# Optimization experiments

Measured on AMD Instinct MI355X. Metric: run time of the kernel, lower is better.

The kernel has to match this reference:

```python
import jax, jax.numpy as jnp
import numpy as np

B, N, F_IN, E_DIM, F, T = 4, 64, 32, 32, 64, 3


def setup_inputs() -> dict:
    key = jax.random.key(0)
    ks = jax.random.split(key, 8)
    X = jax.random.normal(ks[0], (B, N, F_IN), jnp.float32)
    # adjacency mask over the dense N*N ordered-pair layout, broadcast dim 1
    A = (jax.random.uniform(ks[1], (B, N * N, 1)) < 0.25).astype(jnp.float32)
    E = jax.random.normal(ks[2], (B, N * N, E_DIM), jnp.float32)

    def glorot(k, shape):
        fan_in, fan_out = shape
        lim = np.sqrt(6.0 / (fan_in + fan_out)).astype(np.float32)
        return jax.random.uniform(k, shape, jnp.float32, -lim, lim)

    W_embed = glorot(ks[3], (F_IN, F))
    b_embed = jnp.zeros((F,), jnp.float32)
    W_edge = glorot(ks[4], (E_DIM, F * F))
    b_edge = jnp.zeros((F * F,), jnp.float32)
    gru_k = glorot(ks[5], (F, 3 * F))        # input kernel  [F, 3F] (z|r|h)
    gru_rk = glorot(ks[6], (F, 3 * F))       # recurrent kernel
    gru_b = jnp.zeros((3 * F,), jnp.float32)   # input bias
    gru_rb = jnp.zeros((3 * F,), jnp.float32)  # recurrent bias (reset_after)
    return {"X": X, "A": A, "E": E, "W_embed": W_embed, "b_embed": b_embed,
            "W_edge": W_edge, "b_edge": b_edge, "gru_k": gru_k,
            "gru_rk": gru_rk, "gru_b": gru_b, "gru_rb": gru_rb}


def _gru_step(h, x, Wk, Uk, b, rb):
    # Keras GRU cell, reset_after=True: gate order z, r, h
    xg = x @ Wk + b
    hg = h @ Uk + rb
    xz, xr, xh = jnp.split(xg, 3, axis=-1)
    hz, hr, hh = jnp.split(hg, 3, axis=-1)
    z = jax.nn.sigmoid(xz + hz)
    r = jax.nn.sigmoid(xr + hr)
    cand = jnp.tanh(xh + r * hh)
    return z * h + (1.0 - z) * cand


def reference(X, A, E, W_embed, b_embed, W_edge, b_edge,
              gru_k, gru_rk, gru_b, gru_rb):
    H = jax.nn.relu(X @ W_embed + b_embed)            # [B,N,F]
    mask = A.reshape(B, N, N, 1)                      # adjacency mask
    # per-edge transformation matrices (E is constant across T rounds,
    # so the edge MLP is hoisted out of the loop -- same math as original)
    Amat = jax.nn.relu(E @ W_edge + b_edge).reshape(B, N, N, F, F)
    for _ in range(T):
        # message for target i from source j: A_{ij} @ H_j  (batched matvec)
        msgs = jnp.einsum('bnmij,bmj->bnmi', Amat, H)  # [B,N,N,F]
        agg = jnp.sum(msgs * mask, axis=2)             # [B,N,F]
        # GRU over the length-2 sequence [old_state, agg_messages], h0 = 0
        h = jnp.zeros_like(H)
        h = _gru_step(h, H, gru_k, gru_rk, gru_b, gru_rb)
        H = _gru_step(h, agg, gru_k, gru_rk, gru_b, gru_rb)
    return H
```

## Files before the change

kernel.cpp:

```cpp
#include <hip/hip_runtime.h>
#include <math.h>

#define Bv   4
#define Nv   64
#define FIN  32
#define EDIM 32
#define Fv   64
#define NN   (Nv*Nv)
#define ZROW 256

typedef __bf16 bf16x8 __attribute__((ext_vector_type(8)));
typedef float  f32x4  __attribute__((ext_vector_type(4)));

__device__ __forceinline__ float sigmoidf_(float x) {
    return 1.f / (1.f + __expf(-x));
}

__global__ __launch_bounds__(64) void prep_kernel(
    const float* __restrict__ X, const float* __restrict__ W_embed,
    const float* __restrict__ b_embed, const float* __restrict__ A,
    const float* __restrict__ E, const float* __restrict__ W_edge,
    float* __restrict__ H0, float* __restrict__ H1,
    __bf16* __restrict__ Wf, __bf16* __restrict__ Ebf,
    int* __restrict__ ml_g, int* __restrict__ cnt_g)
{
    const int blk  = blockIdx.x;
    const int lane = threadIdx.x;

    if (blk < 256) {
        const int nt = blk;
        const int kb = (lane >> 4) * 8;
        const int c  = nt*16 + (lane & 15);
        bf16x8 v;
        #pragma unroll
        for (int t = 0; t < 8; ++t)
            v[t] = (__bf16)W_edge[(kb + t)*4096 + c];
        *(bf16x8*)(Wf + ((size_t)(nt*64 + lane))*8) = v;
        if (blk == 0) {
            H0[ZROW*Fv + lane] = 0.f;
            H1[ZROW*Fv + lane] = 0.f;
        }
    } else if (blk < 512) {
        const int bn = blk - 256;
        const int b  = bn >> 6;
        const int n  = bn & 63;
        __shared__ int ml[Nv];

        const float av = A[b*NN + n*Nv + lane];
        const unsigned long long mk = __ballot(av != 0.f);
        const int cnt = (int)__popcll(mk);
        if (av != 0.f) {
            const int pos = (int)__popcll(mk & ((1ull << lane) - 1ull));
            ml[pos] = lane;
        }
        __syncthreads();

        ml_g[bn*64 + lane] = (lane < cnt) ? (b*Nv + ml[lane]) : ZROW;
        if (lane == 0) cnt_g[bn] = cnt;

        __bf16 row[EDIM];
        if (lane < cnt) {
            const float* er = E + ((size_t)(b*NN + n*Nv + ml[lane]))*EDIM;
            #pragma unroll
            for (int t = 0; t < 8; ++t) {
                const float4 x = *(const float4*)(er + 4*t);
                row[4*t  ] = (__bf16)x.x; row[4*t+1] = (__bf16)x.y;
                row[4*t+2] = (__bf16)x.z; row[4*t+3] = (__bf16)x.w;
            }
        } else {
            #pragma unroll
            for (int e = 0; e < EDIM; ++e) row[e] = (__bf16)0.f;
        }
        __bf16* dst = Ebf + ((size_t)(bn*64 + lane))*EDIM;
        #pragma unroll
        for (int t = 0; t < 4; ++t)
            *(bf16x8*)(dst + 8*t) = *(bf16x8*)(row + 8*t);
    } else {
        const int bn = blk - 512;
        __shared__ float xs[FIN];
        if (lane < FIN) xs[lane] = X[bn*FIN + lane];
        __syncthreads();
        float acc = b_embed[lane];
        #pragma unroll
        for (int k = 0; k < FIN; ++k)
            acc = fmaf(xs[k], W_embed[k*Fv + lane], acc);
        H0[bn*Fv + lane] = fmaxf(acc, 0.f);
    }
}

template<int MTN>
__device__ __forceinline__ void msg_body(
    int bn, int qq, int w, int lane,
    const float* __restrict__ Hin, const __bf16* __restrict__ Wf,
    const float* __restrict__ b_edge, const __bf16* __restrict__ Ebf,
    const int* __restrict__ ml_g, float* __restrict__ agg_g)
{
    const int c16 = lane & 15;
    const int rg  = (lane >> 4) * 4;
    const int kb  = (lane >> 4) * 8;

    bf16x8 af[MTN];
    int4   ri[MTN];
    #pragma unroll
    for (int mt = 0; mt < MTN; ++mt) {
        af[mt] = *(const bf16x8*)(Ebf + ((size_t)(bn*64 + mt*16 + c16))*EDIM + kb);
        ri[mt] = *(const int4*)(ml_g + bn*64 + mt*16 + rg);
    }

    const int i0 = qq*8 + w*2;
    float p0 = 0.f, p1 = 0.f;

    #pragma unroll
    for (int u = 0; u < 4; ++u) {
        const int jc = u*16 + c16;
        float hu[MTN][4];
        #pragma unroll
        for (int mt = 0; mt < MTN; ++mt) {
            hu[mt][0] = Hin[ri[mt].x*Fv + jc];
            hu[mt][1] = Hin[ri[mt].y*Fv + jc];
            hu[mt][2] = Hin[ri[mt].z*Fv + jc];
            hu[mt][3] = Hin[ri[mt].w*Fv + jc];
        }
        #pragma unroll
        for (int ii = 0; ii < 2; ++ii) {
            const int nt = (i0 + ii)*4 + u;
            const bf16x8 bf = *(const bf16x8*)(Wf + ((size_t)(nt*64 + lane))*8);
            const float  be = b_edge[nt*16 + c16];
            f32x4 cb; cb[0] = be; cb[1] = be; cb[2] = be; cb[3] = be;
            float acc = 0.f;
            #pragma unroll
            for (int mt = 0; mt < MTN; ++mt) {
                f32x4 d = __builtin_amdgcn_mfma_f32_16x16x32_bf16(af[mt], bf, cb, 0, 0, 0);
                acc = fmaf(fmaxf(d[0], 0.f), hu[mt][0], acc);
                acc = fmaf(fmaxf(d[1], 0.f), hu[mt][1], acc);
                acc = fmaf(fmaxf(d[2], 0.f), hu[mt][2], acc);
                acc = fmaf(fmaxf(d[3], 0.f), hu[mt][3], acc);
            }
            if (ii == 0) p0 += acc; else p1 += acc;
        }
    }
    #pragma unroll
    for (int off = 32; off > 0; off >>= 1) {
        p0 += __shfl_xor(p0, off);
        p1 += __shfl_xor(p1, off);
    }
    if (lane == 0) {
        agg_g[bn*Fv + i0]     = p0;
        agg_g[bn*Fv + i0 + 1] = p1;
    }
}

__global__ __launch_bounds__(256) void msg_kernel(
    const float* __restrict__ Hin, const __bf16* __restrict__ Wf,
    const float* __restrict__ b_edge, const __bf16* __restrict__ Ebf,
    const int* __restrict__ ml_g, const int* __restrict__ cnt_g,
    float* __restrict__ agg_g)
{
    const int bn   = blockIdx.x;
    const int qq   = blockIdx.y;
    const int tid  = threadIdx.x;
    const int w    = tid >> 6;
    const int lane = tid & 63;

    const int cnt = cnt_g[bn];
    const int Mt  = (cnt == 0) ? 1 : ((cnt + 15) >> 4);

    if (Mt <= 1) {
        msg_body<1>(bn, qq, w, lane, Hin, Wf, b_edge, Ebf, ml_g, agg_g);
    } else if (Mt == 2) {
        msg_body<2>(bn, qq, w, lane, Hin, Wf, b_edge, Ebf, ml_g, agg_g);
    } else {
        const int c16 = lane & 15;
        const int rg  = (lane >> 4) * 4;
        const int kb  = (lane >> 4) * 8;
        const int i0  = qq*8 + w*2;
        #pragma unroll
        for (int ii = 0; ii < 2; ++ii) {
            float part = 0.f;
            #pragma unroll 1
            for (int u = 0; u < 4; ++u) {
                const int jc = u*16 + c16;
                const int nt = (i0 + ii)*4 + u;
                const bf16x8 bf = *(const bf16x8*)(Wf + ((size_t)(nt*64 + lane))*8);
                const float  be = b_edge[nt*16 + c16];
                f32x4 cb; cb[0] = be; cb[1] = be; cb[2] = be; cb[3] = be;
                for (int mt = 0; mt < Mt; ++mt) {
                    const bf16x8 a_ = *(const bf16x8*)(Ebf + ((size_t)(bn*64 + mt*16 + c16))*EDIM + kb);
                    const int4 ri = *(const int4*)(ml_g + bn*64 + mt*16 + rg);
                    f32x4 d = __builtin_amdgcn_mfma_f32_16x16x32_bf16(a_, bf, cb, 0, 0, 0);
                    part = fmaf(fmaxf(d[0], 0.f), Hin[ri.x*Fv + jc], part);
                    part = fmaf(fmaxf(d[1], 0.f), Hin[ri.y*Fv + jc], part);
                    part = fmaf(fmaxf(d[2], 0.f), Hin[ri.z*Fv + jc], part);
                    part = fmaf(fmaxf(d[3], 0.f), Hin[ri.w*Fv + jc], part);
                }
            }
            #pragma unroll
            for (int off = 32; off > 0; off >>= 1)
                part += __shfl_xor(part, off);
            if (lane == 0) agg_g[bn*Fv + i0 + ii] = part;
        }
    }
}

__global__ __launch_bounds__(192) void gru_kernel(
    const float* __restrict__ Hin, const float* __restrict__ agg_g,
    float* __restrict__ Hout,
    const float* __restrict__ gk, const float* __restrict__ grk,
    const float* __restrict__ gb, const float* __restrict__ grb)
{
    const int bn  = blockIdx.x;
    const int tid = threadIdx.x;

    __shared__ float h_old[Fv];
    __shared__ float aggs[Fv];
    __shared__ float h1[Fv];
    __shared__ float xg[3*Fv];
    __shared__ float hg[3*Fv];

    if (tid < Fv) {
        h_old[tid] = Hin[bn*Fv + tid];
        aggs[tid]  = agg_g[bn*Fv + tid];
    }
    __syncthreads();

    {
        float a0 = 0.f, a1 = 0.f, a2 = 0.f, a3 = 0.f;
        #pragma unroll
        for (int k = 0; k < 16; ++k) {
            a0 = fmaf(h_old[k],      gk[(k     )*192 + tid], a0);
            a1 = fmaf(h_old[k + 16], gk[(k + 16)*192 + tid], a1);
            a2 = fmaf(h_old[k + 32], gk[(k + 32)*192 + tid], a2);
            a3 = fmaf(h_old[k + 48], gk[(k + 48)*192 + tid], a3);
        }
        xg[tid] = gb[tid] + ((a0 + a1) + (a2 + a3));
    }
    __syncthreads();
    if (tid < Fv) {
        float z    = sigmoidf_(xg[tid]       + grb[tid]);
        float r    = sigmoidf_(xg[64 + tid]  + grb[64 + tid]);
        float cand = tanhf    (xg[128 + tid] + r * grb[128 + tid]);
        h1[tid] = (1.f - z) * cand;
    }
    __syncthreads();

    {
        float x0 = 0.f, x1 = 0.f, x2 = 0.f, x3 = 0.f;
        float y0 = 0.f, y1 = 0.f, y2 = 0.f, y3 = 0.f;
        #pragma unroll
        for (int k = 0; k < 16; ++k) {
            x0 = fmaf(aggs[k],      gk [(k     )*192 + tid], x0);
            x1 = fmaf(aggs[k + 16], gk [(k + 16)*192 + tid], x1);
            x2 = fmaf(aggs[k + 32], gk [(k + 32)*192 + tid], x2);
            x3 = fmaf(aggs[k + 48], gk [(k + 48)*192 + tid], x3);
            y0 = fmaf(h1[k],        grk[(k     )*192 + tid], y0);
            y1 = fmaf(h1[k + 16],   grk[(k + 16)*192 + tid], y1);
            y2 = fmaf(h1[k + 32],   grk[(k + 32)*192 + tid], y2);
            y3 = fmaf(h1[k + 48],   grk[(k + 48)*192 + tid], y3);
        }
        xg[tid] = gb[tid]  + ((x0 + x1) + (x2 + x3));
        hg[tid] = grb[tid] + ((y0 + y1) + (y2 + y3));
    }
    __syncthreads();
    if (tid < Fv) {
        float z    = sigmoidf_(xg[tid]       + hg[tid]);
        float r    = sigmoidf_(xg[64 + tid]  + hg[64 + tid]);
        float cand = tanhf    (xg[128 + tid] + r * hg[128 + tid]);
        Hout[bn*Fv + tid] = z * h1[tid] + (1.f - z) * cand;
    }
}

extern "C" void kernel_launch(void* const* d_in, const int* in_sizes, int n_in,
                              void* d_out, int out_size, void* d_ws, size_t ws_size,
                              hipStream_t stream)
{
    const float* X       = (const float*)d_in[0];
    const float* A       = (const float*)d_in[1];
    const float* E       = (const float*)d_in[2];
    const float* W_embed = (const float*)d_in[3];
    const float* b_embed = (const float*)d_in[4];
    const float* W_edge  = (const float*)d_in[5];
    const float* b_edge  = (const float*)d_in[6];
    const float* gk      = (const float*)d_in[7];
    const float* grk     = (const float*)d_in[8];
    const float* gb      = (const float*)d_in[9];
    const float* grb     = (const float*)d_in[10];
    float* out = (float*)d_out;

    float*  H0  = (float*)d_ws;
    float*  H1  = H0 + (ZROW + 1)*Fv;
    __bf16* Wf  = (__bf16*)(H1 + (ZROW + 1)*Fv);
    __bf16* Ebf = Wf + 256*64*8;
    int*    ml_g  = (int*)(Ebf + (size_t)Bv*Nv*64*EDIM);
    int*    cnt_g = ml_g + Bv*Nv*64;

    const dim3 mgrid(Bv*Nv, 8);

    prep_kernel<<<768, 64, 0, stream>>>(X, W_embed, b_embed, A, E, W_edge,
                                        H0, H1, Wf, Ebf, ml_g, cnt_g);

    msg_kernel<<<mgrid, 256, 0, stream>>>(H0, Wf, b_edge, Ebf, ml_g, cnt_g, out);
    gru_kernel<<<Bv*Nv, 192, 0, stream>>>(H0, out, H1, gk, grk, gb, grb);
    msg_kernel<<<mgrid, 256, 0, stream>>>(H1, Wf, b_edge, Ebf, ml_g, cnt_g, out);
    gru_kernel<<<Bv*Nv, 192, 0, stream>>>(H1, out, H0, gk, grk, gb, grb);
    msg_kernel<<<mgrid, 256, 0, stream>>>(H0, Wf, b_edge, Ebf, ml_g, cnt_g, H1);
    gru_kernel<<<Bv*Nv, 192, 0, stream>>>(H0, H1, out, gk, grk, gb, grb);
}
```

Before: 48.09 us.

## Process two nodes per msg block and stage edge-weight fragments in LDS

```diff
diff --git a/kernel.cpp b/kernel.cpp
--- a/kernel.cpp
+++ b/kernel.cpp
@@ -45,7 +45,6 @@
         const int b  = bn >> 6;
         const int n  = bn & 63;
         __shared__ int ml[Nv];
-
         const float av = A[b*NN + n*Nv + lane];
         const unsigned long long mk = __ballot(av != 0.f);
         const int cnt = (int)__popcll(mk);
@@ -54,10 +53,8 @@
             ml[pos] = lane;
         }
         __syncthreads();
-
         ml_g[bn*64 + lane] = (lane < cnt) ? (b*Nv + ml[lane]) : ZROW;
         if (lane == 0) cnt_g[bn] = cnt;
-
         __bf16 row[EDIM];
         if (lane < cnt) {
             const float* er = E + ((size_t)(b*NN + n*Nv + ml[lane]))*EDIM;
@@ -89,9 +86,9 @@
 }
 
 template<int MTN>
-__device__ __forceinline__ void msg_body(
-    int bn, int qq, int w, int lane,
-    const float* __restrict__ Hin, const __bf16* __restrict__ Wf,
+__device__ __forceinline__ void msg_node_lds(
+    int bn, int i0, int lane,
+    const float* __restrict__ Hin, const __bf16* __restrict__ wfl,
     const float* __restrict__ b_edge, const __bf16* __restrict__ Ebf,
     const int* __restrict__ ml_g, float* __restrict__ agg_g)
 {
@@ -107,7 +104,6 @@
         ri[mt] = *(const int4*)(ml_g + bn*64 + mt*16 + rg);
     }
 
-    const int i0 = qq*8 + w*2;
     float p0 = 0.f, p1 = 0.f;
 
     #pragma unroll
@@ -123,8 +119,9 @@
         }
         #pragma unroll
         for (int ii = 0; ii < 2; ++ii) {
-            const int nt = (i0 + ii)*4 + u;
-            const bf16x8 bf = *(const bf16x8*)(Wf + ((size_t)(nt*64 + lane))*8);
+            const int nt  = (i0 + ii)*4 + u;
+            const int ntl = ii*4 + u;
+            const bf16x8 bf = *(const bf16x8*)(wfl + (ntl*64 + lane)*8);
             const float  be = b_edge[nt*16 + c16];
             f32x4 cb; cb[0] = be; cb[1] = be; cb[2] = be; cb[3] = be;
             float acc = 0.f;
@@ -150,56 +147,78 @@
     }
 }
 
+__device__ __forceinline__ void msg_general(
+    int bn, int Mt, int i0, int lane,
+    const float* __restrict__ Hin, const __bf16* __restrict__ Wf,
+    const float* __restrict__ b_edge, const __bf16* __restrict__ Ebf,
+    const int* __restrict__ ml_g, float* __restrict__ agg_g)
+{
+    const int c16 = lane & 15;
+    const int rg  = (lane >> 4) * 4;
+    const int kb  = (lane >> 4) * 8;
+    #pragma unroll
+    for (int ii = 0; ii < 2; ++ii) {
+        float part = 0.f;
+        #pragma unroll 1
+        for (int u = 0; u < 4; ++u) {
+            const int jc = u*16 + c16;
+            const int nt = (i0 + ii)*4 + u;
+            const bf16x8 bf = *(const bf16x8*)(Wf + ((size_t)(nt*64 + lane))*8);
+            const float  be = b_edge[nt*16 + c16];
+            f32x4 cb; cb[0] = be; cb[1] = be; cb[2] = be; cb[3] = be;
+            for (int mt = 0; mt < Mt; ++mt) {
+                const bf16x8 a_ = *(const bf16x8*)(Ebf + ((size_t)(bn*64 + mt*16 + c16))*EDIM + kb);
+                const int4 ri = *(const int4*)(ml_g + bn*64 + mt*16 + rg);
+                f32x4 d = __builtin_amdgcn_mfma_f32_16x16x32_bf16(a_, bf, cb, 0, 0, 0);
+                part = fmaf(fmaxf(d[0], 0.f), Hin[ri.x*Fv + jc], part);
+                part = fmaf(fmaxf(d[1], 0.f), Hin[ri.y*Fv + jc], part);
+                part = fmaf(fmaxf(d[2], 0.f), Hin[ri.z*Fv + jc], part);
+                part = fmaf(fmaxf(d[3], 0.f), Hin[ri.w*Fv + jc], part);
+            }
+        }
+        #pragma unroll
+        for (int off = 32; off > 0; off >>= 1)
+            part += __shfl_xor(part, off);
+        if (lane == 0) agg_g[bn*Fv + i0 + ii] = part;
+    }
+}
+
 __global__ __launch_bounds__(256) void msg_kernel(
     const float* __restrict__ Hin, const __bf16* __restrict__ Wf,
     const float* __restrict__ b_edge, const __bf16* __restrict__ Ebf,
     const int* __restrict__ ml_g, const int* __restrict__ cnt_g,
     float* __restrict__ agg_g)
 {
-    const int bn   = blockIdx.x;
+    const int g    = blockIdx.x;
     const int qq   = blockIdx.y;
     const int tid  = threadIdx.x;
     const int w    = tid >> 6;
     const int lane = tid & 63;
 
-    const int cnt = cnt_g[bn];
-    const int Mt  = (cnt == 0) ? 1 : ((cnt + 15) >> 4);
-
-    if (Mt <= 1) {
-        msg_body<1>(bn, qq, w, lane, Hin, Wf, b_edge, Ebf, ml_g, agg_g);
-    } else if (Mt == 2) {
-        msg_body<2>(bn, qq, w, lane, Hin, Wf, b_edge, Ebf, ml_g, agg_g);
-    } else {
-        const int c16 = lane & 15;
-        const int rg  = (lane >> 4) * 4;
-        const int kb  = (lane >> 4) * 8;
-        const int i0  = qq*8 + w*2;
-        #pragma unroll
-        for (int ii = 0; ii < 2; ++ii) {
-            float part = 0.f;
-            #pragma unroll 1
-            for (int u = 0; u < 4; ++u) {
-                const int jc = u*16 + c16;
-                const int nt = (i0 + ii)*4 + u;
-                const bf16x8 bf = *(const bf16x8*)(Wf + ((size_t)(nt*64 + lane))*8);
-                const float  be = b_edge[nt*16 + c16];
-                f32x4 cb; cb[0] = be; cb[1] = be; cb[2] = be; cb[3] = be;
-                for (int mt = 0; mt < Mt; ++mt) {
-                    const bf16x8 a_ = *(const bf16x8*)(Ebf + ((size_t)(bn*64 + mt*16 + c16))*EDIM + kb);
-                    const int4 ri = *(const int4*)(ml_g + bn*64 + mt*16 + rg);
-                    f32x4 d = __builtin_amdgcn_mfma_f32_16x16x32_bf16(a_, bf, cb, 0, 0, 0);
-                    part = fmaf(fmaxf(d[0], 0.f), Hin[ri.x*Fv + jc], part);
-                    part = fmaf(fmaxf(d[1], 0.f), Hin[ri.y*Fv + jc], part);
-                    part = fmaf(fmaxf(d[2], 0.f), Hin[ri.z*Fv + jc], part);
-                    part = fmaf(fmaxf(d[3], 0.f), Hin[ri.w*Fv + jc], part);
-                }
-            }
-            #pragma unroll
-            for (int off = 32; off > 0; off >>= 1)
-                part += __shfl_xor(part, off);
-            if (lane == 0) agg_g[bn*Fv + i0 + ii] = part;
-        }
-    }
+    __shared__ __bf16 wfl[4][8][64*8];
+
+    const int i0  = qq*8 + w*2;
+    const int bn0 = g*2, bn1 = g*2 + 1;
+
+    #pragma unroll
+    for (int ntl = 0; ntl < 8; ++ntl) {
+        const int nt = (i0 + (ntl >> 2))*4 + (ntl & 3);
+        *(bf16x8*)(&wfl[w][ntl][lane*8]) =
+            *(const bf16x8*)(Wf + ((size_t)(nt*64 + lane))*8);
+    }
+    const __bf16* wflw = &wfl[w][0][0];
+
+    const int c0 = cnt_g[bn0];
+    const int Mt0 = (c0 == 0) ? 1 : ((c0 + 15) >> 4);
+    if (Mt0 <= 1)      msg_node_lds<1>(bn0, i0, lane, Hin, wflw, b_edge, Ebf, ml_g, agg_g);
+    else if (Mt0 == 2) msg_node_lds<2>(bn0, i0, lane, Hin, wflw, b_edge, Ebf, ml_g, agg_g);
+    else               msg_general(bn0, Mt0, i0, lane, Hin, Wf, b_edge, Ebf, ml_g, agg_g);
+
+    const int c1 = cnt_g[bn1];
+    const int Mt1 = (c1 == 0) ? 1 : ((c1 + 15) >> 4);
+    if (Mt1 <= 1)      msg_node_lds<1>(bn1, i0, lane, Hin, wflw, b_edge, Ebf, ml_g, agg_g);
+    else if (Mt1 == 2) msg_node_lds<2>(bn1, i0, lane, Hin, wflw, b_edge, Ebf, ml_g, agg_g);
+    else               msg_general(bn1, Mt1, i0, lane, Hin, Wf, b_edge, Ebf, ml_g, agg_g);
 }
 
 __global__ __launch_bounds__(192) void gru_kernel(
@@ -293,7 +312,7 @@
     int*    ml_g  = (int*)(Ebf + (size_t)Bv*Nv*64*EDIM);
     int*    cnt_g = ml_g + Bv*Nv*64;
 
-    const dim3 mgrid(Bv*Nv, 8);
+    const dim3 mgrid(Bv*Nv/2, 8);
 
     prep_kernel<<<768, 64, 0, stream>>>(X, W_embed, b_embed, A, E, W_edge,
                                         H0, H1, Wf, Ebf, ml_g, cnt_g);
```

Measured after the change: 59.03 us. 22.7% more time.

## Fuse message and GRU kernels per round via last-block atomic counter

Applied to the files above, without the earlier changes.

```diff
diff --git a/kernel.cpp b/kernel.cpp
--- a/kernel.cpp
+++ b/kernel.cpp
@@ -8,6 +8,7 @@
 #define Fv   64
 #define NN   (Nv*Nv)
 #define ZROW 256
+#define SCOPE_AGENT __HIP_MEMORY_SCOPE_AGENT
 
 typedef __bf16 bf16x8 __attribute__((ext_vector_type(8)));
 typedef float  f32x4  __attribute__((ext_vector_type(4)));
@@ -22,7 +23,8 @@
     const float* __restrict__ E, const float* __restrict__ W_edge,
     float* __restrict__ H0, float* __restrict__ H1,
     __bf16* __restrict__ Wf, __bf16* __restrict__ Ebf,
-    int* __restrict__ ml_g, int* __restrict__ cnt_g)
+    int* __restrict__ ml_g, int* __restrict__ cnt_g,
+    int* __restrict__ cnt2)
 {
     const int blk  = blockIdx.x;
     const int lane = threadIdx.x;
@@ -45,7 +47,6 @@
         const int b  = bn >> 6;
         const int n  = bn & 63;
         __shared__ int ml[Nv];
-
         const float av = A[b*NN + n*Nv + lane];
         const unsigned long long mk = __ballot(av != 0.f);
         const int cnt = (int)__popcll(mk);
@@ -54,10 +55,9 @@
             ml[pos] = lane;
         }
         __syncthreads();
-
         ml_g[bn*64 + lane] = (lane < cnt) ? (b*Nv + ml[lane]) : ZROW;
         if (lane == 0) cnt_g[bn] = cnt;
-
+        if (lane < 3)  cnt2[lane*256 + bn] = 0;
         __bf16 row[EDIM];
         if (lane < cnt) {
             const float* er = E + ((size_t)(b*NN + n*Nv + ml[lane]))*EDIM;
@@ -145,16 +145,57 @@
         p1 += __shfl_xor(p1, off);
     }
     if (lane == 0) {
-        agg_g[bn*Fv + i0]     = p0;
-        agg_g[bn*Fv + i0 + 1] = p1;
-    }
-}
-
-__global__ __launch_bounds__(256) void msg_kernel(
+        __hip_atomic_store(&agg_g[bn*Fv + i0],     p0, __ATOMIC_RELAXED, SCOPE_AGENT);
+        __hip_atomic_store(&agg_g[bn*Fv + i0 + 1], p1, __ATOMIC_RELAXED, SCOPE_AGENT);
+    }
+}
+
+__device__ __forceinline__ void msg_general(
+    int bn, int Mt, int qq, int w, int lane,
     const float* __restrict__ Hin, const __bf16* __restrict__ Wf,
     const float* __restrict__ b_edge, const __bf16* __restrict__ Ebf,
-    const int* __restrict__ ml_g, const int* __restrict__ cnt_g,
-    float* __restrict__ agg_g)
+    const int* __restrict__ ml_g, float* __restrict__ agg_g)
+{
+    const int c16 = lane & 15;
+    const int rg  = (lane >> 4) * 4;
+    const int kb  = (lane >> 4) * 8;
+    const int i0  = qq*8 + w*2;
+    #pragma unroll
+    for (int ii = 0; ii < 2; ++ii) {
+        float part = 0.f;
+        #pragma unroll 1
+        for (int u = 0; u < 4; ++u) {
+            const int jc = u*16 + c16;
+            const int nt = (i0 + ii)*4 + u;
+            const bf16x8 bf = *(const bf16x8*)(Wf + ((size_t)(nt*64 + lane))*8);
+            const float  be = b_edge[nt*16 + c16];
+            f32x4 cb; cb[0] = be; cb[1] = be; cb[2] = be; cb[3] = be;
+            for (int mt = 0; mt < Mt; ++mt) {
+                const bf16x8 a_ = *(const bf16x8*)(Ebf + ((size_t)(bn*64 + mt*16 + c16))*EDIM + kb);
+                const int4 ri = *(const int4*)(ml_g + bn*64 + mt*16 + rg);
+                f32x4 d = __builtin_amdgcn_mfma_f32_16x16x32_bf16(a_, bf, cb, 0, 0, 0);
+                part = fmaf(fmaxf(d[0], 0.f), Hin[ri.x*Fv + jc], part);
+                part = fmaf(fmaxf(d[1], 0.f), Hin[ri.y*Fv + jc], part);
+                part = fmaf(fmaxf(d[2], 0.f), Hin[ri.z*Fv + jc], part);
+                part = fmaf(fmaxf(d[3], 0.f), Hin[ri.w*Fv + jc], part);
+            }
+        }
+        #pragma unroll
+        for (int off = 32; off > 0; off >>= 1)
+            part += __shfl_xor(part, off);
+        if (lane == 0)
+            __hip_atomic_store(&agg_g[bn*Fv + i0 + ii], part, __ATOMIC_RELAXED, SCOPE_AGENT);
+    }
+}
+
+__global__ __launch_bounds__(256) void round_kernel(
+    const float* __restrict__ Hin, float* __restrict__ Hout,
+    const __bf16* __restrict__ Wf, const float* __restrict__ b_edge,
+    const __bf16* __restrict__ Ebf, const int* __restrict__ ml_g,
+    const int* __restrict__ cnt_g,
+    const float* __restrict__ gk, const float* __restrict__ grk,
+    const float* __restrict__ gb, const float* __restrict__ grb,
+    float* __restrict__ agg_g, int* __restrict__ cnt2)
 {
     const int bn   = blockIdx.x;
     const int qq   = blockIdx.y;
@@ -164,52 +205,17 @@
 
     const int cnt = cnt_g[bn];
     const int Mt  = (cnt == 0) ? 1 : ((cnt + 15) >> 4);
-
-    if (Mt <= 1) {
-        msg_body<1>(bn, qq, w, lane, Hin, Wf, b_edge, Ebf, ml_g, agg_g);
-    } else if (Mt == 2) {
-        msg_body<2>(bn, qq, w, lane, Hin, Wf, b_edge, Ebf, ml_g, agg_g);
-    } else {
-        const int c16 = lane & 15;
-        const int rg  = (lane >> 4) * 4;
-        const int kb  = (lane >> 4) * 8;
-        const int i0  = qq*8 + w*2;
-        #pragma unroll
-        for (int ii = 0; ii < 2; ++ii) {
-            float part = 0.f;
-            #pragma unroll 1
-            for (int u = 0; u < 4; ++u) {
-                const int jc = u*16 + c16;
-                const int nt = (i0 + ii)*4 + u;
-                const bf16x8 bf = *(const bf16x8*)(Wf + ((size_t)(nt*64 + lane))*8);
-                const float  be = b_edge[nt*16 + c16];
-                f32x4 cb; cb[0] = be; cb[1] = be; cb[2] = be; cb[3] = be;
-                for (int mt = 0; mt < Mt; ++mt) {
-                    const bf16x8 a_ = *(const bf16x8*)(Ebf + ((size_t)(bn*64 + mt*16 + c16))*EDIM + kb);
-                    const int4 ri = *(const int4*)(ml_g + bn*64 + mt*16 + rg);
-                    f32x4 d = __builtin_amdgcn_mfma_f32_16x16x32_bf16(a_, bf, cb, 0, 0, 0);
-                    part = fmaf(fmaxf(d[0], 0.f), Hin[ri.x*Fv + jc], part);
-                    part = fmaf(fmaxf(d[1], 0.f), Hin[ri.y*Fv + jc], part);
-                    part = fmaf(fmaxf(d[2], 0.f), Hin[ri.z*Fv + jc], part);
-                    part = fmaf(fmaxf(d[3], 0.f), Hin[ri.w*Fv + jc], part);
-                }
-            }
-            #pragma unroll
-            for (int off = 32; off > 0; off >>= 1)
-                part += __shfl_xor(part, off);
-            if (lane == 0) agg_g[bn*Fv + i0 + ii] = part;
-        }
-    }
-}
-
-__global__ __launch_bounds__(192) void gru_kernel(
-    const float* __restrict__ Hin, const float* __restrict__ agg_g,
-    float* __restrict__ Hout,
-    const float* __restrict__ gk, const float* __restrict__ grk,
-    const float* __restrict__ gb, const float* __restrict__ grb)
-{
-    const int bn  = blockIdx.x;
-    const int tid = threadIdx.x;
+    if (Mt <= 1)      msg_body<1>(bn, qq, w, lane, Hin, Wf, b_edge, Ebf, ml_g, agg_g);
+    else if (Mt == 2) msg_body<2>(bn, qq, w, lane, Hin, Wf, b_edge, Ebf, ml_g, agg_g);
+    else              msg_general(bn, Mt, qq, w, lane, Hin, Wf, b_edge, Ebf, ml_g, agg_g);
+
+    __syncthreads();
+
+    __shared__ int old_sh;
+    if (tid == 0)
+        old_sh = __hip_atomic_fetch_add(&cnt2[bn], 1, __ATOMIC_ACQ_REL, SCOPE_AGENT);
+    __syncthreads();
+    if (old_sh != 7) return;
 
     __shared__ float h_old[Fv];
     __shared__ float aggs[Fv];
@@ -219,11 +225,11 @@
 
     if (tid < Fv) {
         h_old[tid] = Hin[bn*Fv + tid];
-        aggs[tid]  = agg_g[bn*Fv + tid];
-    }
-    __syncthreads();
-
-    {
+        aggs[tid]  = __hip_atomic_load(&agg_g[bn*Fv + tid], __ATOMIC_RELAXED, SCOPE_AGENT);
+    }
+    __syncthreads();
+
+    if (tid < 3*Fv) {
         float a0 = 0.f, a1 = 0.f, a2 = 0.f, a3 = 0.f;
         #pragma unroll
         for (int k = 0; k < 16; ++k) {
@@ -242,8 +248,7 @@
         h1[tid] = (1.f - z) * cand;
     }
     __syncthreads();
-
-    {
+    if (tid < 3*Fv) {
         float x0 = 0.f, x1 = 0.f, x2 = 0.f, x3 = 0.f;
         float y0 = 0.f, y1 = 0.f, y2 = 0.f, y3 = 0.f;
         #pragma unroll
@@ -292,16 +297,18 @@
     __bf16* Ebf = Wf + 256*64*8;
     int*    ml_g  = (int*)(Ebf + (size_t)Bv*Nv*64*EDIM);
     int*    cnt_g = ml_g + Bv*Nv*64;
-
-    const dim3 mgrid(Bv*Nv, 8);
+    int*    cnt2  = cnt_g + Bv*Nv;
+    float*  agg_g = (float*)(cnt2 + 3*256);
+
+    const dim3 rgrid(Bv*Nv, 8);
 
     prep_kernel<<<768, 64, 0, stream>>>(X, W_embed, b_embed, A, E, W_edge,
-                                        H0, H1, Wf, Ebf, ml_g, cnt_g);
-
-    msg_kernel<<<mgrid, 256, 0, stream>>>(H0, Wf, b_edge, Ebf, ml_g, cnt_g, out);
-    gru_kernel<<<Bv*Nv, 192, 0, stream>>>(H0, out, H1, gk, grk, gb, grb);
-    msg_kernel<<<mgrid, 256, 0, stream>>>(H1, Wf, b_edge, Ebf, ml_g, cnt_g, out);
-    gru_kernel<<<Bv*Nv, 192, 0, stream>>>(H1, out, H0, gk, grk, gb, grb);
-    msg_kernel<<<mgrid, 256, 0, stream>>>(H0, Wf, b_edge, Ebf, ml_g, cnt_g, H1);
-    gru_kernel<<<Bv*Nv, 192, 0, stream>>>(H0, H1, out, gk, grk, gb, grb);
-}
+                                        H0, H1, Wf, Ebf, ml_g, cnt_g, cnt2);
+
+    round_kernel<<<rgrid, 256, 0, stream>>>(H0, H1, Wf, b_edge, Ebf, ml_g, cnt_g,
+                                            gk, grk, gb, grb, agg_g, cnt2 + 0);
+    round_kernel<<<rgrid, 256, 0, stream>>>(H1, H0, Wf, b_edge, Ebf, ml_g, cnt_g,
+                                            gk, grk, gb, grb, agg_g, cnt2 + 256);
+    round_kernel<<<rgrid, 256, 0, stream>>>(H0, out, Wf, b_edge, Ebf, ml_g, cnt_g,
+                                            gk, grk, gb, grb, agg_g, cnt2 + 512);
+}
```

After: 134.6 us. +179.9%, slower.
